# Optimization experiments

Hardware: AMD Instinct MI355X
Metric: run time of the kernel (lower is better)

Reference implementation:

```python
import jax, jax.numpy as jnp
import numpy as np

B, T, V, E, H = 4, 2048, 50257, 1024, 16
D = E // H  # head dim = 64

def _ln(x, g, b, eps=1e-5):
    mu = jnp.mean(x, axis=-1, keepdims=True)
    var = jnp.var(x, axis=-1, keepdims=True)
    return (x - mu) * jax.lax.rsqrt(var + eps) * g + b

def setup_inputs() -> dict:
    key = jax.random.key(0)
    ks = jax.random.split(key, 20)
    s = 0.02
    return {
        "ids": jax.random.randint(ks[0], (B, T), 0, V),
        "wte": jax.random.normal(ks[1], (V, E), jnp.float32) * s,
        "wpe": jax.random.normal(ks[2], (T, E), jnp.float32) * s,
        "wq": jax.random.normal(ks[3], (H, E, D), jnp.float32) * s,
        "wk": jax.random.normal(ks[4], (H, E, D), jnp.float32) * s,
        "wv": jax.random.normal(ks[5], (H, E, D), jnp.float32) * s,
        "bq": jnp.zeros((H, D), jnp.float32),
        "bk": jnp.zeros((H, D), jnp.float32),
        "bv": jnp.zeros((H, D), jnp.float32),
        "wproj": jax.random.normal(ks[6], (E, E), jnp.float32) * s,
        "bproj": jnp.zeros((E,), jnp.float32),
        "ln1_g": jnp.ones((E,), jnp.float32),
        "ln1_b": jnp.zeros((E,), jnp.float32),
        "ln2_g": jnp.ones((E,), jnp.float32),
        "ln2_b": jnp.zeros((E,), jnp.float32),
        "w_fc": jax.random.normal(ks[7], (E, 4 * E), jnp.float32) * s,
        "b_fc": jnp.zeros((4 * E,), jnp.float32),
        "w_out": jax.random.normal(ks[8], (4 * E, E), jnp.float32) * s,
        "b_out": jnp.zeros((E,), jnp.float32),
    }

def reference(ids, wte, wpe, wq, wk, wv, bq, bk, bv, wproj, bproj,
              ln1_g, ln1_b, ln2_g, ln2_b, w_fc, b_fc, w_out, b_out):
    t = ids.shape[1]
    x = wte[ids] + wpe[:t]                      # [B,T,E]
    # --- attention (all heads batched; faithful per-head math) ---
    h = _ln(x, ln1_g, ln1_b)
    q = jnp.einsum('btc,hcd->bhtd', h, wq) + bq[None, :, None, :]
    k = jnp.einsum('btc,hcd->bhtd', h, wk) + bk[None, :, None, :]
    v = jnp.einsum('btc,hcd->bhtd', h, wv) + bv[None, :, None, :]
    scores = jnp.einsum('bhtd,bhsd->bhts', q, k) * (1.0 / np.sqrt(D))
    causal = jnp.tril(jnp.ones((t, t), bool))
    scores = jnp.where(causal, scores, -jnp.inf)
    attn = jax.nn.softmax(scores, axis=-1)      # dropout = identity (eval)
    o = jnp.einsum('bhts,bhsd->bhtd', attn, v)
    o = jnp.transpose(o, (0, 2, 1, 3)).reshape(x.shape[0], t, E)  # concat heads
    x = x + o @ wproj + bproj
    # --- MLP ---
    h2 = _ln(x, ln2_g, ln2_b)
    m = jax.nn.gelu(h2 @ w_fc + b_fc, approximate=False) @ w_out + b_out
    return x + m
```

## Files before the change

kernel.cpp:

```cpp
#include <hip/hip_runtime.h>
#include <math.h>

#define BB 4
#define TT 2048
#define EE 1024
#define HH 16
#define DD 64
#define MM (BB*TT)

typedef unsigned short u16;
typedef __bf16 bf16x8 __attribute__((ext_vector_type(8)));
typedef float  f32x4  __attribute__((ext_vector_type(4)));

__device__ inline float bf2f(u16 u){ union{unsigned int i; float f;} v; v.i=((unsigned int)u)<<16; return v.f; }
__device__ inline u16 f2bf(float f){ union{float f; unsigned int i;} v; v.f=f; return (u16)((v.i + 0x7fffu + ((v.i>>16)&1u))>>16); }

__device__ inline void gload_lds16(const void* g, void* l){
  __builtin_amdgcn_global_load_lds((__attribute__((address_space(1))) void*)g,
                                   (__attribute__((address_space(3))) void*)l, 16, 0, 0);
}

__global__ __launch_bounds__(256) void transpose_tile(
    const float* __restrict__ W, u16* __restrict__ WT, int N, int K)
{
    __shared__ float t[32][33];
    const int n0 = blockIdx.x*32, k0 = blockIdx.y*32;
    const int tx = threadIdx.x, ty = threadIdx.y;
    #pragma unroll
    for (int j=0;j<4;j++)
        t[ty + j*8][tx] = W[(size_t)(k0 + ty + j*8)*N + n0 + tx];
    __syncthreads();
    #pragma unroll
    for (int j=0;j<4;j++)
        WT[(size_t)(n0 + ty + j*8)*K + k0 + tx] = f2bf(t[tx][ty + j*8]);
}

__global__ __launch_bounds__(256) void transpose_v(
    const u16* __restrict__ V, u16* __restrict__ VT)
{
    __shared__ u16 t[32][34];
    const int bh = blockIdx.z;
    const int t0 = blockIdx.x*32;
    const int d0 = blockIdx.y*32;
    const int tx = threadIdx.x, ty = threadIdx.y;
    const u16* Vb = V + (size_t)bh*TT*DD;
    u16* VTb = VT + (size_t)bh*TT*DD;
    #pragma unroll
    for (int j=0;j<4;j++)
        t[ty+j*8][tx] = Vb[(size_t)(t0+ty+j*8)*DD + d0+tx];
    __syncthreads();
    #pragma unroll
    for (int j=0;j<4;j++)
        VTb[(size_t)(d0+ty+j*8)*TT + t0+tx] = t[tx][ty+j*8];
}

__global__ __launch_bounds__(256) void repack_qkv_tiled(
    const float* __restrict__ wq, const float* __restrict__ wk, const float* __restrict__ wv,
    u16* __restrict__ WT)
{
    __shared__ float t[32][33];
    const int z = blockIdx.z, which = z>>4, hh = z&15;
    const int d0 = blockIdx.x*32, c0 = blockIdx.y*32;
    const int tx = threadIdx.x, ty = threadIdx.y;
    const float* w = which==0 ? wq : (which==1 ? wk : wv);
    #pragma unroll
    for (int j=0;j<4;j++)
        t[ty + j*8][tx] = w[((size_t)hh*EE + c0 + ty + j*8)*DD + d0 + tx];
    __syncthreads();
    #pragma unroll
    for (int j=0;j<4;j++)
        WT[(size_t)(which*1024 + hh*64 + d0 + ty + j*8)*1024 + c0 + tx] = f2bf(t[tx][ty + j*8]);
}

__global__ __launch_bounds__(256) void copy_bias_qkv(
    const float* __restrict__ bq, const float* __restrict__ bk, const float* __restrict__ bv,
    float* __restrict__ bias)
{
    int i = blockIdx.x*256 + threadIdx.x;
    const float* b = i<1024 ? bq : (i<2048 ? bk : bv);
    bias[i] = b[i & 1023];
}

__global__ __launch_bounds__(256) void embed_ln1(
    const int* __restrict__ ids, const float* __restrict__ wte, const float* __restrict__ wpe,
    const float* __restrict__ g, const float* __restrict__ b,
    float* __restrict__ x_out, u16* __restrict__ h_out)
{
    const int token = blockIdx.x;
    const int t = token & (TT-1);
    const int id = ids[token];
    const int tid = threadIdx.x;
    float vals[4]; float s=0.f, s2=0.f;
    #pragma unroll
    for (int i=0;i<4;i++){
        int e = tid + i*256;
        float v = wte[(size_t)id*EE + e] + wpe[(size_t)t*EE + e];
        vals[i]=v; s+=v; s2+=v*v;
    }
    for (int off=32; off>=1; off>>=1){ s += __shfl_xor(s,off); s2 += __shfl_xor(s2,off); }
    __shared__ float red[8];
    int wave=tid>>6, lane=tid&63;
    if (lane==0){ red[wave]=s; red[4+wave]=s2; }
    __syncthreads();
    s = red[0]+red[1]+red[2]+red[3];
    s2 = red[4]+red[5]+red[6]+red[7];
    float mu = s*(1.f/EE);
    float var = s2*(1.f/EE) - mu*mu;
    float rstd = rsqrtf(var + 1e-5f);
    #pragma unroll
    for (int i=0;i<4;i++){
        int e = tid + i*256; float v = vals[i];
        x_out[(size_t)token*EE + e] = v;
        h_out[(size_t)token*EE + e] = f2bf((v-mu)*rstd*g[e] + b[e]);
    }
}

__global__ __launch_bounds__(256) void ln_fwd(
    const float* __restrict__ xin, const float* __restrict__ g, const float* __restrict__ b,
    u16* __restrict__ hout)
{
    const int token = blockIdx.x;
    const int tid = threadIdx.x;
    float vals[4]; float s=0.f, s2=0.f;
    #pragma unroll
    for (int i=0;i<4;i++){
        int e = tid + i*256;
        float v = xin[(size_t)token*EE + e];
        vals[i]=v; s+=v; s2+=v*v;
    }
    for (int off=32; off>=1; off>>=1){ s += __shfl_xor(s,off); s2 += __shfl_xor(s2,off); }
    __shared__ float red[8];
    int wave=tid>>6, lane=tid&63;
    if (lane==0){ red[wave]=s; red[4+wave]=s2; }
    __syncthreads();
    s = red[0]+red[1]+red[2]+red[3];
    s2 = red[4]+red[5]+red[6]+red[7];
    float mu = s*(1.f/EE);
    float var = s2*(1.f/EE) - mu*mu;
    float rstd = rsqrtf(var + 1e-5f);
    #pragma unroll
    for (int i=0;i<4;i++){
        int e = tid + i*256; float v = vals[i];
        hout[(size_t)token*EE + e] = f2bf((v-mu)*rstd*g[e] + b[e]);
    }
}

template<int MODE>
__global__ __launch_bounds__(256) void gemm_bt(
    const u16* __restrict__ A, const u16* __restrict__ BT, const float* __restrict__ bias,
    float* CoutF, const float* resid, u16* __restrict__ CoutH,
    u16* __restrict__ q_out, u16* __restrict__ k_out, u16* __restrict__ v_out,
    int Ndim, int Kdim)
{
    __shared__ u16 As[128*32];
    __shared__ u16 Bs[128*32];
    const int tid = threadIdx.x, wave = tid>>6, lane = tid&63;
    const int quad = lane>>4, l16 = lane&15;
    const int m0 = blockIdx.x<<7, n0 = blockIdx.y<<7;
    const int wm = (wave>>1)<<6, wn = (wave&1)<<6;
    const f32x4 zf = {0.f,0.f,0.f,0.f};
    f32x4 acc[4][4];
    #pragma unroll
    for (int i=0;i<4;i++)
        #pragma unroll
        for (int j=0;j<4;j++) acc[i][j]=zf;

    const int rA = lane>>2;
    const int kA = (lane&3)*8;
    for (int k0=0; k0<Kdim; k0+=32){
        __syncthreads();
        #pragma unroll
        for (int i=0;i<2;i++){
            const int inst = wave*2+i;
            const int row  = inst*16 + rA;
            gload_lds16(A  + (size_t)(m0+row)*Kdim + k0 + kA, &As[inst*512]);
            gload_lds16(BT + (size_t)(n0+row)*Kdim + k0 + kA, &Bs[inst*512]);
        }
        __syncthreads();
        bf16x8 af[4], bfr[4];
        #pragma unroll
        for (int mt=0;mt<4;mt++) af[mt]  = *(const bf16x8*)&As[(wm + mt*16 + l16)*32 + quad*8];
        #pragma unroll
        for (int nt=0;nt<4;nt++) bfr[nt] = *(const bf16x8*)&Bs[(wn + nt*16 + l16)*32 + quad*8];
        #pragma unroll
        for (int mt=0;mt<4;mt++)
            #pragma unroll
            for (int nt=0;nt<4;nt++)
                acc[mt][nt] = __builtin_amdgcn_mfma_f32_16x16x32_bf16(af[mt], bfr[nt], acc[mt][nt], 0, 0, 0);
    }
    #pragma unroll
    for (int mt=0;mt<4;mt++){
        #pragma unroll
        for (int nt=0;nt<4;nt++){
            #pragma unroll
            for (int r=0;r<4;r++){
                int m = m0 + wm + mt*16 + quad*4 + r;
                int n = n0 + wn + nt*16 + l16;
                float v = acc[mt][nt][r] + bias[n];
                if (MODE==0){
                    int which = n>>10, hd = n&1023, hh = hd>>6, d = hd&63;
                    u16* dst = which==0 ? q_out : (which==1 ? k_out : v_out);
                    int bb = m>>11, t = m&(TT-1);
                    dst[(((size_t)(bb*HH+hh)*TT + t)<<6) + d] = f2bf(v);
                } else if (MODE==1){
                    size_t idx = (size_t)m*Ndim + n;
                    CoutF[idx] = resid[idx] + v;
                } else {
                    size_t idx = (size_t)m*Ndim + n;
                    CoutH[idx] = f2bf(0.5f*v*(1.0f + erff(v*0.70710678118f)));
                }
            }
        }
    }
}

__global__ __launch_bounds__(256) void attn_kernel(
    const u16* __restrict__ Q, const u16* __restrict__ K, const u16* __restrict__ VT,
    u16* __restrict__ O)
{
    __shared__ u16 Ks[64*64];
    __shared__ u16 Vs[64*64];
    __shared__ u16 Ps[4*32*64];
    const int tid = threadIdx.x, wave = tid>>6, lane = tid&63;
    const int quad = lane>>4, l16 = lane&15;
    const int qt0 = blockIdx.x*128, bh = blockIdx.y;
    const size_t base = (size_t)bh*TT*DD;
    const u16* Qb = Q + base;
    const u16* Kb = K + base;
    const u16* VTb = VT + base;
    const int q0 = qt0 + wave*32;

    bf16x8 qf[2][2];
    #pragma unroll
    for (int m=0;m<2;m++)
        #pragma unroll
        for (int h2=0;h2<2;h2++)
            qf[m][h2] = *(const bf16x8*)&Qb[(size_t)(q0+m*16+l16)*DD + h2*32 + quad*8];

    const f32x4 zf = {0.f,0.f,0.f,0.f};
    f32x4 oacc[2][4];
    float lsum[2][4];
    #pragma unroll
    for (int m=0;m<2;m++){
        #pragma unroll
        for (int dt=0;dt<4;dt++) oacc[m][dt]=zf;
        #pragma unroll
        for (int r=0;r<4;r++) lsum[m][r]=0.f;
    }

    const int ktEnd = (q0+31)>>6;
    const int ktMax = (qt0+127)>>6;

    const int c0 = wave*64 + lane, c1 = 256 + wave*64 + lane;
    const int r0 = c0>>3, j0 = (c0&7) ^ (r0&7);
    const int r1 = c1>>3, j1 = (c1&7) ^ (r1&7);

    for (int kt=0; kt<=ktMax; kt++){
        __syncthreads();
        {
            const int s0 = kt*64;
            gload_lds16(Kb  + (size_t)(s0+r0)*DD + j0*8, &Ks[wave*512]);
            gload_lds16(Kb  + (size_t)(s0+r1)*DD + j1*8, &Ks[(4+wave)*512]);
            gload_lds16(VTb + (size_t)r0*TT + s0 + j0*8, &Vs[wave*512]);
            gload_lds16(VTb + (size_t)r1*TT + s0 + j1*8, &Vs[(4+wave)*512]);
        }
        __syncthreads();
        if (kt > ktEnd) continue;

        f32x4 a[2][4];
        #pragma unroll
        for (int m=0;m<2;m++)
            #pragma unroll
            for (int st=0;st<4;st++) a[m][st]=zf;
        #pragma unroll
        for (int h2=0;h2<2;h2++){
            #pragma unroll
            for (int st=0;st<4;st++){
                const int s = st*16 + l16;
                const int jc = h2*4 + quad;
                bf16x8 kf = *(const bf16x8*)&Ks[s*64 + (jc ^ (s&7))*8];
                #pragma unroll
                for (int m=0;m<2;m++)
                    a[m][st] = __builtin_amdgcn_mfma_f32_16x16x32_bf16(qf[m][h2], kf, a[m][st], 0,0,0);
            }
        }
        #pragma unroll
        for (int m=0;m<2;m++){
            const int q0m = q0 + m*16;
            #pragma unroll
            for (int st=0;st<4;st++){
                #pragma unroll
                for (int r=0;r<4;r++){
                    const int qrow = q0m + quad*4 + r;
                    const int s = kt*64 + st*16 + l16;
                    float p = (s > qrow) ? 0.f
                            : exp2f(fminf(a[m][st][r]*0.1803369f, 40.f));
                    lsum[m][r] += p;
                    const int ql = m*16 + quad*4 + r;
                    const int sc3 = st*2 + (l16>>3);
                    Ps[wave*2048 + ql*64 + (sc3 ^ (ql&7))*8 + (l16&7)] = f2bf(p);
                }
            }
        }
        #pragma unroll
        for (int kh=0; kh<2; kh++){
            const int jc = kh*4 + quad;
            bf16x8 pf[2];
            #pragma unroll
            for (int m=0;m<2;m++){
                const int ql16 = m*16 + l16;
                pf[m] = *(const bf16x8*)&Ps[wave*2048 + ql16*64 + (jc ^ (ql16&7))*8];
            }
            #pragma unroll
            for (int dt=0; dt<4; dt++){
                const int d = dt*16 + l16;
                bf16x8 vf = *(const bf16x8*)&Vs[d*64 + (jc ^ (d&7))*8];
                #pragma unroll
                for (int m=0;m<2;m++)
                    oacc[m][dt] = __builtin_amdgcn_mfma_f32_16x16x32_bf16(pf[m], vf, oacc[m][dt], 0,0,0);
            }
        }
    }
    #pragma unroll
    for (int off=1; off<16; off<<=1)
        #pragma unroll
        for (int m=0;m<2;m++)
            #pragma unroll
            for (int r=0;r<4;r++)
                lsum[m][r] += __shfl_xor(lsum[m][r], off);

    const int bb = bh>>4, hh = bh&15;
    #pragma unroll
    for (int m=0;m<2;m++)
        #pragma unroll
        for (int dt=0;dt<4;dt++)
            #pragma unroll
            for (int r=0;r<4;r++){
                const int t = q0 + m*16 + quad*4 + r;
                const float o = oacc[m][dt][r] / lsum[m][r];
                O[(size_t)(bb*TT + t)*EE + hh*64 + dt*16 + l16] = f2bf(o);
            }
}

extern "C" void kernel_launch(void* const* d_in, const int* in_sizes, int n_in,
                              void* d_out, int out_size, void* d_ws, size_t ws_size,
                              hipStream_t stream)
{
    (void)in_sizes; (void)n_in; (void)out_size; (void)ws_size;
    const int*   ids  = (const int*)d_in[0];
    const float* wte  = (const float*)d_in[1];
    const float* wpe  = (const float*)d_in[2];
    const float* wq   = (const float*)d_in[3];
    const float* wk   = (const float*)d_in[4];
    const float* wv   = (const float*)d_in[5];
    const float* bq   = (const float*)d_in[6];
    const float* bk   = (const float*)d_in[7];
    const float* bv   = (const float*)d_in[8];
    const float* wproj= (const float*)d_in[9];
    const float* bproj= (const float*)d_in[10];
    const float* ln1g = (const float*)d_in[11];
    const float* ln1b = (const float*)d_in[12];
    const float* ln2g = (const float*)d_in[13];
    const float* ln2b = (const float*)d_in[14];
    const float* wfc  = (const float*)d_in[15];
    const float* bfc  = (const float*)d_in[16];
    const float* wout = (const float*)d_in[17];
    const float* bout = (const float*)d_in[18];

    const size_t MTOK = (size_t)MM*EE;
    char* p = (char*)d_ws;
    float* x    = (float*)p;  p += MTOK*sizeof(float);
    u16*  h     = (u16*)p;    p += MTOK*sizeof(u16);
    u16*  Qb    = (u16*)p;    p += MTOK*sizeof(u16);
    u16*  Kb    = (u16*)p;    p += MTOK*sizeof(u16);
    u16*  Vb    = (u16*)p;    p += MTOK*sizeof(u16);
    u16*  Ob    = (u16*)p;    p += MTOK*sizeof(u16);
    u16*  fcact = Qb;
    u16*  VTv   = h;
    u16*  WqkvT = (u16*)p;    p += (size_t)3072*1024*sizeof(u16);
    float* biasq= (float*)p;  p += 3072*sizeof(float);
    u16*  wprojT= (u16*)p;    p += (size_t)1024*1024*sizeof(u16);
    u16*  wfcT  = (u16*)p;    p += (size_t)4096*1024*sizeof(u16);
    u16*  woutT = (u16*)p;    p += (size_t)1024*4096*sizeof(u16);
    float* out  = (float*)d_out;

    repack_qkv_tiled<<<dim3(2,32,48),dim3(32,8),0,stream>>>(wq,wk,wv,WqkvT);
    copy_bias_qkv<<<12,256,0,stream>>>(bq,bk,bv,biasq);
    transpose_tile<<<dim3(32,32), dim3(32,8),0,stream>>>(wproj, wprojT, 1024, 1024);
    transpose_tile<<<dim3(128,32),dim3(32,8),0,stream>>>(wfc,   wfcT,   4096, 1024);
    transpose_tile<<<dim3(32,128),dim3(32,8),0,stream>>>(wout,  woutT,  1024, 4096);
    embed_ln1<<<MM,256,0,stream>>>(ids, wte, wpe, ln1g, ln1b, x, h);
    gemm_bt<0><<<dim3(64,24),256,0,stream>>>(h, WqkvT, biasq, nullptr,nullptr,nullptr, Qb,Kb,Vb, 3072, 1024);
    transpose_v<<<dim3(64,2,64),dim3(32,8),0,stream>>>(Vb, VTv);
    attn_kernel<<<dim3(TT/128, BB*HH),256,0,stream>>>(Qb,Kb,VTv,Ob);
    gemm_bt<1><<<dim3(64,8),256,0,stream>>>(Ob, wprojT, bproj, x, x, nullptr, nullptr,nullptr,nullptr, 1024, 1024);
    ln_fwd<<<MM,256,0,stream>>>(x, ln2g, ln2b, h);
    gemm_bt<2><<<dim3(64,32),256,0,stream>>>(h, wfcT, bfc, nullptr,nullptr, fcact, nullptr,nullptr,nullptr, 4096, 1024);
    gemm_bt<1><<<dim3(64,8),256,0,stream>>>(fcact, woutT, bout, out, x, nullptr, nullptr,nullptr,nullptr, 1024, 4096);
}
```

Measured before the change: 846.9 us.

## Pair causal attention query tiles per block to balance work and share K/V loads

Each attention block now handles two 128-row query tiles (pair and 15-pair) of the same head. This balances the causal triangle so every block does equal work, and lets both tiles reuse one staged K/V tile. The grid is remapped to 512 blocks with a bh-interleaved ordering, and launch bounds request 2 blocks per SM. It also skips the mask computation on fully unmasked tiles and truncates P to bf16 instead of rounding, at some precision cost and with higher register pressure.

Result: faster. 757.7 us (-10.5%).

```diff
diff --git a/kernel.cpp b/kernel.cpp
--- a/kernel.cpp
+++ b/kernel.cpp
@@ -14,6 +14,7 @@
 
 __device__ inline float bf2f(u16 u){ union{unsigned int i; float f;} v; v.i=((unsigned int)u)<<16; return v.f; }
 __device__ inline u16 f2bf(float f){ union{float f; unsigned int i;} v; v.f=f; return (u16)((v.i + 0x7fffu + ((v.i>>16)&1u))>>16); }
+__device__ inline u16 f2bf_trunc(float f){ union{float f; unsigned int i;} v; v.f=f; return (u16)(v.i>>16); }
 
 __device__ inline void gload_lds16(const void* g, void* l){
   __builtin_amdgcn_global_load_lds((__attribute__((address_space(1))) void*)g,
@@ -214,42 +215,113 @@
     }
 }
 
-__global__ __launch_bounds__(256) void attn_kernel(
+__device__ __forceinline__ void attn_proc_tile(
+    int kt, int q0, int quad, int l16,
+    const u16* Ks, const u16* Vs, u16* Psw,
+    const bf16x8 (&qf)[2][2], f32x4 (&oacc)[2][4], float (&lsum)[2][4])
+{
+    if (kt > ((q0+31)>>6)) return;
+    const f32x4 zf = {0.f,0.f,0.f,0.f};
+    f32x4 a[2][4];
+    #pragma unroll
+    for (int m=0;m<2;m++)
+        #pragma unroll
+        for (int st=0;st<4;st++) a[m][st]=zf;
+    #pragma unroll
+    for (int h2=0;h2<2;h2++){
+        #pragma unroll
+        for (int st=0;st<4;st++){
+            const int s = st*16 + l16;
+            const int jc = h2*4 + quad;
+            bf16x8 kf = *(const bf16x8*)&Ks[s*64 + (jc ^ (s&7))*8];
+            #pragma unroll
+            for (int m=0;m<2;m++)
+                a[m][st] = __builtin_amdgcn_mfma_f32_16x16x32_bf16(qf[m][h2], kf, a[m][st], 0,0,0);
+        }
+    }
+    const bool needMask = (kt*64 + 63 > q0);
+    #pragma unroll
+    for (int m=0;m<2;m++){
+        const int q0m = q0 + m*16;
+        #pragma unroll
+        for (int st=0;st<4;st++){
+            #pragma unroll
+            for (int r=0;r<4;r++){
+                float p = exp2f(fminf(a[m][st][r]*0.1803369f, 40.f));
+                if (needMask){
+                    const int qrow = q0m + quad*4 + r;
+                    const int s = kt*64 + st*16 + l16;
+                    if (s > qrow) p = 0.f;
+                }
+                lsum[m][r] += p;
+                const int ql = m*16 + quad*4 + r;
+                const int sc3 = st*2 + (l16>>3);
+                Psw[ql*64 + (sc3 ^ (ql&7))*8 + (l16&7)] = f2bf_trunc(p);
+            }
+        }
+    }
+    #pragma unroll
+    for (int kh=0; kh<2; kh++){
+        const int jc = kh*4 + quad;
+        bf16x8 pf[2];
+        #pragma unroll
+        for (int m=0;m<2;m++){
+            const int ql16 = m*16 + l16;
+            pf[m] = *(const bf16x8*)&Psw[ql16*64 + (jc ^ (ql16&7))*8];
+        }
+        #pragma unroll
+        for (int dt=0; dt<4; dt++){
+            const int d = dt*16 + l16;
+            bf16x8 vf = *(const bf16x8*)&Vs[d*64 + (jc ^ (d&7))*8];
+            #pragma unroll
+            for (int m=0;m<2;m++)
+                oacc[m][dt] = __builtin_amdgcn_mfma_f32_16x16x32_bf16(pf[m], vf, oacc[m][dt], 0,0,0);
+        }
+    }
+}
+
+__global__ __launch_bounds__(256,2) void attn_kernel(
     const u16* __restrict__ Q, const u16* __restrict__ K, const u16* __restrict__ VT,
     u16* __restrict__ O)
 {
     __shared__ u16 Ks[64*64];
     __shared__ u16 Vs[64*64];
-    __shared__ u16 Ps[4*32*64];
+    __shared__ u16 Ps[4*2048];
     const int tid = threadIdx.x, wave = tid>>6, lane = tid&63;
     const int quad = lane>>4, l16 = lane&15;
-    const int qt0 = blockIdx.x*128, bh = blockIdx.y;
+    const int id = blockIdx.x;
+    const int bh   = (id&7) | ((id>>6)<<3);
+    const int pair = (id>>3)&7;
+    const int qtA = pair, qtB = 15-pair;
     const size_t base = (size_t)bh*TT*DD;
     const u16* Qb = Q + base;
     const u16* Kb = K + base;
     const u16* VTb = VT + base;
-    const int q0 = qt0 + wave*32;
-
-    bf16x8 qf[2][2];
+    const int qA0 = qtA*128 + wave*32;
+    const int qB0 = qtB*128 + wave*32;
+    u16* Psw = &Ps[wave*2048];
+
+    bf16x8 qfA[2][2], qfB[2][2];
     #pragma unroll
     for (int m=0;m<2;m++)
         #pragma unroll
-        for (int h2=0;h2<2;h2++)
-            qf[m][h2] = *(const bf16x8*)&Qb[(size_t)(q0+m*16+l16)*DD + h2*32 + quad*8];
+        for (int h2=0;h2<2;h2++){
+            qfA[m][h2] = *(const bf16x8*)&Qb[(size_t)(qA0+m*16+l16)*DD + h2*32 + quad*8];
+            qfB[m][h2] = *(const bf16x8*)&Qb[(size_t)(qB0+m*16+l16)*DD + h2*32 + quad*8];
+        }
 
     const f32x4 zf = {0.f,0.f,0.f,0.f};
-    f32x4 oacc[2][4];
-    float lsum[2][4];
+    f32x4 oaccA[2][4], oaccB[2][4];
+    float lsumA[2][4], lsumB[2][4];
     #pragma unroll
     for (int m=0;m<2;m++){
         #pragma unroll
-        for (int dt=0;dt<4;dt++) oacc[m][dt]=zf;
-        #pragma unroll
-        for (int r=0;r<4;r++) lsum[m][r]=0.f;
-    }
-
-    const int ktEnd = (q0+31)>>6;
-    const int ktMax = (qt0+127)>>6;
+        for (int dt=0;dt<4;dt++){ oaccA[m][dt]=zf; oaccB[m][dt]=zf; }
+        #pragma unroll
+        for (int r=0;r<4;r++){ lsumA[m][r]=0.f; lsumB[m][r]=0.f; }
+    }
+
+    const int ktMax = 31 - 2*pair;
 
     const int c0 = wave*64 + lane, c1 = 256 + wave*64 + lane;
     const int r0 = c0>>3, j0 = (c0&7) ^ (r0&7);
@@ -265,69 +337,19 @@
             gload_lds16(VTb + (size_t)r1*TT + s0 + j1*8, &Vs[(4+wave)*512]);
         }
         __syncthreads();
-        if (kt > ktEnd) continue;
-
-        f32x4 a[2][4];
+        attn_proc_tile(kt, qB0, quad, l16, Ks, Vs, Psw, qfB, oaccB, lsumB);
+        attn_proc_tile(kt, qA0, quad, l16, Ks, Vs, Psw, qfA, oaccA, lsumA);
+    }
+
+    #pragma unroll
+    for (int off=1; off<16; off<<=1)
         #pragma unroll
         for (int m=0;m<2;m++)
             #pragma unroll
-            for (int st=0;st<4;st++) a[m][st]=zf;
-        #pragma unroll
-        for (int h2=0;h2<2;h2++){
-            #pragma unroll
-            for (int st=0;st<4;st++){
-                const int s = st*16 + l16;
-                const int jc = h2*4 + quad;
-                bf16x8 kf = *(const bf16x8*)&Ks[s*64 + (jc ^ (s&7))*8];
-                #pragma unroll
-                for (int m=0;m<2;m++)
-                    a[m][st] = __builtin_amdgcn_mfma_f32_16x16x32_bf16(qf[m][h2], kf, a[m][st], 0,0,0);
+            for (int r=0;r<4;r++){
+                lsumA[m][r] += __shfl_xor(lsumA[m][r], off);
+                lsumB[m][r] += __shfl_xor(lsumB[m][r], off);
             }
-        }
-        #pragma unroll
-        for (int m=0;m<2;m++){
-            const int q0m = q0 + m*16;
-            #pragma unroll
-            for (int st=0;st<4;st++){
-                #pragma unroll
-                for (int r=0;r<4;r++){
-                    const int qrow = q0m + quad*4 + r;
-                    const int s = kt*64 + st*16 + l16;
-                    float p = (s > qrow) ? 0.f
-                            : exp2f(fminf(a[m][st][r]*0.1803369f, 40.f));
-                    lsum[m][r] += p;
-                    const int ql = m*16 + quad*4 + r;
-                    const int sc3 = st*2 + (l16>>3);
-                    Ps[wave*2048 + ql*64 + (sc3 ^ (ql&7))*8 + (l16&7)] = f2bf(p);
-                }
-            }
-        }
-        #pragma unroll
-        for (int kh=0; kh<2; kh++){
-            const int jc = kh*4 + quad;
-            bf16x8 pf[2];
-            #pragma unroll
-            for (int m=0;m<2;m++){
-                const int ql16 = m*16 + l16;
-                pf[m] = *(const bf16x8*)&Ps[wave*2048 + ql16*64 + (jc ^ (ql16&7))*8];
-            }
-            #pragma unroll
-            for (int dt=0; dt<4; dt++){
-                const int d = dt*16 + l16;
-                bf16x8 vf = *(const bf16x8*)&Vs[d*64 + (jc ^ (d&7))*8];
-                #pragma unroll
-                for (int m=0;m<2;m++)
-                    oacc[m][dt] = __builtin_amdgcn_mfma_f32_16x16x32_bf16(pf[m], vf, oacc[m][dt], 0,0,0);
-            }
-        }
-    }
-    #pragma unroll
-    for (int off=1; off<16; off<<=1)
-        #pragma unroll
-        for (int m=0;m<2;m++)
-            #pragma unroll
-            for (int r=0;r<4;r++)
-                lsum[m][r] += __shfl_xor(lsum[m][r], off);
 
     const int bb = bh>>4, hh = bh&15;
     #pragma unroll
@@ -336,9 +358,10 @@
         for (int dt=0;dt<4;dt++)
             #pragma unroll
             for (int r=0;r<4;r++){
-                const int t = q0 + m*16 + quad*4 + r;
-                const float o = oacc[m][dt][r] / lsum[m][r];
-                O[(size_t)(bb*TT + t)*EE + hh*64 + dt*16 + l16] = f2bf(o);
+                int t = qA0 + m*16 + quad*4 + r;
+                O[(size_t)(bb*TT + t)*EE + hh*64 + dt*16 + l16] = f2bf(oaccA[m][dt][r] / lsumA[m][r]);
+                t = qB0 + m*16 + quad*4 + r;
+                O[(size_t)(bb*TT + t)*EE + hh*64 + dt*16 + l16] = f2bf(oaccB[m][dt][r] / lsumB[m][r]);
             }
 }
 
@@ -392,7 +415,7 @@
     embed_ln1<<<MM,256,0,stream>>>(ids, wte, wpe, ln1g, ln1b, x, h);
     gemm_bt<0><<<dim3(64,24),256,0,stream>>>(h, WqkvT, biasq, nullptr,nullptr,nullptr, Qb,Kb,Vb, 3072, 1024);
     transpose_v<<<dim3(64,2,64),dim3(32,8),0,stream>>>(Vb, VTv);
-    attn_kernel<<<dim3(TT/128, BB*HH),256,0,stream>>>(Qb,Kb,VTv,Ob);
+    attn_kernel<<<512,256,0,stream>>>(Qb,Kb,VTv,Ob);
     gemm_bt<1><<<dim3(64,8),256,0,stream>>>(Ob, wprojT, bproj, x, x, nullptr, nullptr,nullptr,nullptr, 1024, 1024);
     ln_fwd<<<MM,256,0,stream>>>(x, ln2g, ln2b, h);
     gemm_bt<2><<<dim3(64,32),256,0,stream>>>(h, wfcT, bfc, nullptr,nullptr, fcact, nullptr,nullptr,nullptr, 4096, 1024);
```
